# Kernel tuning notes

Measured on AMD Instinct MI355X. Metric: run time of the kernel, lower is better.

The kernel has to match this reference:

```python
import jax, jax.numpy as jnp
import numpy as np
from jax import lax

B_SZ = 2
EMBED = 384          # d_model == d_inner (expand=1)
DEPTH = 12
DSTATE = 16
DCONV = 4
DTRANK = 24          # ceil(384/16)
GH, GW, GD = 16, 8, 8
PH, PW, PD = 16, 32, 8
L = GH * GW * GD            # 1024 tokens
PATCH_DIM = PH * PW * PD    # 4096


def setup_inputs() -> dict:
    key = jax.random.key(0)
    ks = jax.random.split(key, 12)
    d = EMBED
    return {
        "x": jax.random.normal(ks[0], (B_SZ, 1, GH * PH, GW * PW, GD * PD), dtype=jnp.float32),
        "batch_params": jax.random.uniform(ks[1], (B_SZ, 4), minval=0.1, maxval=1.0),
        "patch_w": jax.random.normal(ks[2], (PATCH_DIM, d)) * 0.02,
        "patch_b": jnp.zeros((d,), jnp.float32),
        "in_proj_w": jax.random.normal(ks[3], (DEPTH, d, 2 * d)) * 0.02,
        "conv_w": jax.random.normal(ks[4], (DEPTH, d, DCONV)) * 0.1,
        "conv_b": jnp.zeros((DEPTH, d), jnp.float32),
        "x_proj_w": jax.random.normal(ks[5], (DEPTH, d, DTRANK + 2 * DSTATE)) * 0.02,
        "dt_proj_w": jax.random.normal(ks[6], (DEPTH, DTRANK, d)) * 0.02,
        "dt_proj_b": jnp.full((DEPTH, d), -4.6, jnp.float32),  # softplus(-4.6) ~ 0.01 init dt
        "A_log": jnp.log(jnp.tile(jnp.arange(1, DSTATE + 1, dtype=jnp.float32), (DEPTH, EMBED, 1))),
        "Dskip": jnp.ones((DEPTH, d), jnp.float32),
        "out_proj_w": jax.random.normal(ks[7], (DEPTH, d, d)) * 0.02,
        "norm_w": jnp.ones((DEPTH, d), jnp.float32),
        "norm_b": jnp.zeros((DEPTH, d), jnp.float32),
        "final_norm_w": jnp.ones((d,), jnp.float32),
        "final_norm_b": jnp.zeros((d,), jnp.float32),
        "has_velocity_mask": jnp.array([True, False]),
    }


def _layernorm(h, w, b, eps=1e-5):
    mu = h.mean(-1, keepdims=True)
    var = ((h - mu) ** 2).mean(-1, keepdims=True)
    return (h - mu) / jnp.sqrt(var + eps) * w + b


def _physical_coords(batch_params, mask):
    # grid indices -> physical (distance, angle, velocity/time), [B, L, 3]
    h = jnp.arange(GH, dtype=jnp.float32)[None, :, None, None]
    w = jnp.arange(GW, dtype=jnp.float32)[None, None, :, None]
    dd = jnp.arange(GD, dtype=jnp.float32)[None, None, None, :]
    rr = batch_params[:, 0][:, None, None, None]
    ar = batch_params[:, 1][:, None, None, None]
    vr = batch_params[:, 2][:, None, None, None]
    B = batch_params.shape[0]
    shape = (B, GH, GW, GD)
    dist = jnp.broadcast_to(h * rr, shape)
    angle = jnp.broadcast_to((w - GW / 2) * ar, shape)
    m = mask[:, None, None, None]
    vel = jnp.broadcast_to(jnp.where(m, (dd - GD / 2) * vr, dd * vr), shape)
    coords = jnp.stack([dist, angle, vel], axis=-1).reshape(B, -1, 3)
    # PIPE normalization
    d0 = coords[:, :, 0]
    dmax = jnp.max(d0, 1, keepdims=True)
    n0 = d0 / jnp.where(dmax == 0, 1.0, dmax)
    a = coords[:, :, 1]
    amax = jnp.max(jnp.abs(a), 1, keepdims=True)
    n1 = a / jnp.where(amax == 0, 1.0, amax)
    v = coords[:, :, 2]
    vam = jnp.max(jnp.abs(v), 1, keepdims=True)
    vam = jnp.where(vam == 0, 1.0, vam)
    vm = jnp.max(v, 1, keepdims=True)
    vm = jnp.where(vm == 0, 1.0, vm)
    n2 = jnp.where(mask[:, None], v / vam, v / vm)
    return jnp.stack([n0, n1, n2], axis=-1)


def _pos_embed(coords):
    # embed_dim % 3 == 0 and per-coord dim even -> pure sin/cos blocks
    dpc = EMBED // 3
    omega = 1.0 / (10000.0 ** (jnp.arange(dpc // 2, dtype=jnp.float32) / (dpc / 2.0)))
    embs = []
    for j in range(3):
        out = coords[:, :, j, None] * omega          # [B, L, dpc//2]
        embs.append(jnp.concatenate([jnp.sin(out), jnp.cos(out)], axis=-1))
    return jnp.concatenate(embs, axis=-1)            # [B, L, EMBED]


def _forward(x, batch_params, patch_w, patch_b, in_proj_w, conv_w, conv_b,
             x_proj_w, dt_proj_w, dt_proj_b, A_log, Dskip, out_proj_w,
             norm_w, norm_b, final_norm_w, final_norm_b, has_velocity_mask):
    B = x.shape[0]
    # 3D patch embed (conv3d with stride == kernel == patch) as reshape + GEMM
    xp = x[:, 0].reshape(B, GH, PH, GW, PW, GD, PD)
    xp = xp.transpose(0, 1, 3, 5, 2, 4, 6).reshape(B, L, PATCH_DIM)
    tok = xp @ patch_w + patch_b                     # [B, L, EMBED]
    coords = _physical_coords(batch_params, has_velocity_mask)
    tok = tok + _pos_embed(coords)

    def mamba_layer(tok, params):
        ipw, cw, cb, xpw, dtw, dtb, Al, Dp, opw, nw, nb = params
        h = _layernorm(tok, nw, nb)
        xz = h @ ipw                                  # [B, L, 2d]
        xi, z = jnp.split(xz, 2, axis=-1)
        # depthwise causal conv1d (kernel DCONV) + silu
        xc = lax.conv_general_dilated(
            xi.transpose(0, 2, 1), cw[:, None, :], (1,), [(DCONV - 1, 0)],
            feature_group_count=EMBED, dimension_numbers=("NCH", "OIH", "NCH"))
        xc = jax.nn.silu(xc + cb[:, None]).transpose(0, 2, 1)   # [B, L, d]
        dbl = xc @ xpw
        dt = jax.nn.softplus(dbl[..., :DTRANK] @ dtw + dtb)     # [B, L, d]
        Bm = dbl[..., DTRANK:DTRANK + DSTATE]                   # [B, L, N]
        Cm = dbl[..., DTRANK + DSTATE:]                         # [B, L, N]
        A = -jnp.exp(Al)                                        # [d, N]

        def step(hst, inps):
            dt_t, B_t, C_t, u_t = inps                          # [B,d],[B,N],[B,N],[B,d]
            dA = jnp.exp(dt_t[:, :, None] * A)                  # [B, d, N]
            hst = hst * dA + (dt_t * u_t)[:, :, None] * B_t[:, None, :]
            return hst, jnp.einsum("bdn,bn->bd", hst, C_t)

        h0 = jnp.zeros((B, EMBED, DSTATE), tok.dtype)
        _, ys = lax.scan(step, h0, (dt.transpose(1, 0, 2), Bm.transpose(1, 0, 2),
                                    Cm.transpose(1, 0, 2), xc.transpose(1, 0, 2)))
        y = ys.transpose(1, 0, 2) + xc * Dp
        y = y * jax.nn.silu(z)
        return tok + y @ opw, None

    tok, _ = lax.scan(mamba_layer, tok,
                      (in_proj_w, conv_w, conv_b, x_proj_w, dt_proj_w, dt_proj_b,
                       A_log, Dskip, out_proj_w, norm_w, norm_b))
    return _layernorm(tok, final_norm_w, final_norm_b)


def reference(x, batch_params, patch_w, patch_b, in_proj_w, conv_w, conv_b,
              x_proj_w, dt_proj_w, dt_proj_b, A_log, Dskip, out_proj_w,
              norm_w, norm_b, final_norm_w, final_norm_b, has_velocity_mask):
    return _forward(x, batch_params, patch_w, patch_b, in_proj_w, conv_w, conv_b,
                    x_proj_w, dt_proj_w, dt_proj_b, A_log, Dskip, out_proj_w,
                    norm_w, norm_b, final_norm_w, final_norm_b, has_velocity_mask)
```

## Files before the change

kernel.cpp:

```cpp
#include <hip/hip_runtime.h>


#define NTOK 2048

typedef short bf16x8 __attribute__((ext_vector_type(8)));
typedef float f32x4 __attribute__((ext_vector_type(4)));
typedef unsigned short us4 __attribute__((ext_vector_type(4)));

__device__ __forceinline__ float bf2f(unsigned short u) {
    return __uint_as_float(((unsigned)u) << 16);
}
__device__ __forceinline__ unsigned short f2bf(float f) {
    unsigned u = __float_as_uint(f);
    u += 0x7fffu + ((u >> 16) & 1u);
    return (unsigned short)(u >> 16);
}
__device__ __forceinline__ float siluf(float x) { return x / (1.f + expf(-x)); }

__device__ __forceinline__ float ldr(const void* p, size_t i, int bf) {
    if (bf) return bf2f(((const unsigned short*)p)[i]);
    return ((const float*)p)[i];
}
template<int BF>
__device__ __forceinline__ float ld(const void* p, size_t i) {
    if (BF) return bf2f(((const unsigned short*)p)[i]);
    return ((const float*)p)[i];
}

__global__ void detect_kernel(const void* dskip, int* flag) {
    flag[0] = (((const unsigned short*)dskip)[0] == 0x3F80u) ? 1 : 0;
}

__global__ __launch_bounds__(256)
void transposeP_kernel(const int* flag, const void* pw, unsigned short* wtP)
{
    __shared__ unsigned short Ts[32 * 36];
    const int bid = blockIdx.x;
    const int kb = bid / 12, nb = bid % 12;
    const int tid = threadIdx.x;
    const int r = tid >> 3, c0 = (tid & 7) * 4;
    const int BF = *flag;
#pragma unroll
    for (int i = 0; i < 4; i++) {
        size_t si = (size_t)(kb * 32 + r) * 384 + nb * 32 + c0 + i;
        Ts[(c0 + i) * 36 + r] = f2bf(ldr(pw, si, BF));
    }
    __syncthreads();
    *(us4*)(wtP + (size_t)(nb * 32 + r) * 4096 + kb * 32 + c0) = *(const us4*)&Ts[r * 36 + c0];
}

__global__ __launch_bounds__(256)
void transposeL_kernel(const int* flag, const void* ipw, const void* opw, int lyr,
                       unsigned short* wtL, unsigned short* wtOl)
{
    __shared__ unsigned short Ts[32 * 36];
    const int bid = blockIdx.x;
    const void* src; size_t soff; unsigned short* dst; int N, kb, nb;
    if (bid < 288) {
        src = ipw; soff = (size_t)lyr * 294912; dst = wtL; N = 768;
        kb = bid / 24; nb = bid % 24;
    } else {
        int rel = bid - 288;
        src = opw; soff = (size_t)lyr * 147456; dst = wtOl; N = 384;
        kb = rel / 12; nb = rel % 12;
    }
    const int tid = threadIdx.x;
    const int r = tid >> 3, c0 = (tid & 7) * 4;
    const int BF = *flag;
#pragma unroll
    for (int i = 0; i < 4; i++) {
        size_t si = soff + (size_t)(kb * 32 + r) * N + nb * 32 + c0 + i;
        Ts[(c0 + i) * 36 + r] = f2bf(ldr(src, si, BF));
    }
    __syncthreads();
    *(us4*)(dst + (size_t)(nb * 32 + r) * 384 + kb * 32 + c0) = *(const us4*)&Ts[r * 36 + c0];
}

__global__ __launch_bounds__(256)
void transposeAll_kernel(const int* flag, const void* ipw, const void* opw,
                         unsigned short* wtL12, unsigned short* wtO12)
{
    __shared__ unsigned short Ts[32 * 36];
    const int lyr = blockIdx.y;
    const int bid = blockIdx.x;
    const void* src; size_t soff; unsigned short* dst; int N, kb, nb;
    if (bid < 288) {
        src = ipw; soff = (size_t)lyr * 294912;
        dst = wtL12 + (size_t)lyr * 294912; N = 768;
        kb = bid / 24; nb = bid % 24;
    } else {
        int rel = bid - 288;
        src = opw; soff = (size_t)lyr * 147456;
        dst = wtO12 + (size_t)lyr * 147456; N = 384;
        kb = rel / 12; nb = rel % 12;
    }
    const int tid = threadIdx.x;
    const int r = tid >> 3, c0 = (tid & 7) * 4;
    const int BF = *flag;
#pragma unroll
    for (int i = 0; i < 4; i++) {
        size_t si = soff + (size_t)(kb * 32 + r) * N + nb * 32 + c0 + i;
        Ts[(c0 + i) * 36 + r] = f2bf(ldr(src, si, BF));
    }
    __syncthreads();
    *(us4*)(dst + (size_t)(nb * 32 + r) * 384 + kb * 32 + c0) = *(const us4*)&Ts[r * 36 + c0];
}

template<int MODE>
__global__ __launch_bounds__(256)
void gemm_kernel(const unsigned short* __restrict__ A,
                 const unsigned short* __restrict__ WT,
                 void* __restrict__ out0, unsigned short* __restrict__ out1)
{
    const int mtile = blockIdx.x;
    const int ntile = blockIdx.y;
    const int tid = threadIdx.x;
    const int w = tid >> 6, lane = tid & 63;
    const int l15 = lane & 15, quad = lane >> 4;
    const int mbase = mtile * 32;
    const int nbase = ntile * 64 + w * 16;
    f32x4 acc0 = {0.f,0.f,0.f,0.f}, acc1 = acc0;
    const bf16x8* Ap0 = (const bf16x8*)(A + (size_t)(mbase + l15) * 384 + quad * 8);
    const bf16x8* Ap1 = (const bf16x8*)(A + (size_t)(mbase + 16 + l15) * 384 + quad * 8);
    const bf16x8* Bp  = (const bf16x8*)(WT + (size_t)(nbase + l15) * 384 + quad * 8);
    const int nkt = (MODE == 1) ? 6 : 12;
    const int kt0 = (MODE == 1) ? blockIdx.z * 6 : 0;
#pragma unroll
    for (int ki = 0; ki < nkt; ki++) {
        const int kt = kt0 + ki;
        bf16x8 a0 = Ap0[kt * 4];
        bf16x8 a1 = Ap1[kt * 4];
        bf16x8 b  = Bp[kt * 4];
        acc0 = __builtin_amdgcn_mfma_f32_16x16x32_bf16(a0, b, acc0, 0, 0, 0);
        acc1 = __builtin_amdgcn_mfma_f32_16x16x32_bf16(a1, b, acc1, 0, 0, 0);
    }
    f32x4 accs[2] = {acc0, acc1};
#pragma unroll
    for (int mi = 0; mi < 2; mi++)
#pragma unroll
    for (int r = 0; r < 4; r++) {
        int m = mbase + mi * 16 + quad * 4 + r;
        int n = nbase + l15;
        float v = accs[mi][r];
        if (MODE == 0) {
            if (n < 384) ((unsigned short*)out0)[(size_t)m * 384 + n] = f2bf(v);
            else out1[(size_t)m * 384 + (n - 384)] = f2bf(siluf(v));
        } else {
            atomicAdd(&((float*)out0)[(size_t)m * 384 + n], v);
        }
    }
}

template<int BF>
__device__ void posinit_body(const void* __restrict__ pb, const void* __restrict__ bparams,
                             const unsigned char* __restrict__ maskp, float* __restrict__ tok)
{
    const int gid = blockIdx.x * 256 + threadIdx.x;
    const int t = gid / 384;
    const int n = gid - t * 384;
    const int b = t >> 10, l = t & 1023;
    const int gh = l >> 6, gw = (l >> 3) & 7, gd = l & 7;
    const int j = n >> 7;
    const int ii = n & 127;
    const int i0 = (ii < 64) ? ii : ii - 64;
    const float omega = exp2f(-(float)i0 * 0.20762050593046014f);
    float rr = ld<BF>(bparams, b * 4 + 0);
    float ar = ld<BF>(bparams, b * 4 + 1);
    float vr = ld<BF>(bparams, b * 4 + 2);
    bool mk = maskp[b] != 0;
    float cj;
    if (j == 0) {
        float dmax = (rr >= 0.f) ? 15.f * rr : 0.f;
        if (dmax == 0.f) dmax = 1.f;
        cj = (float)gh * rr / dmax;
    } else if (j == 1) {
        float amax = 4.f * fabsf(ar);
        if (amax == 0.f) amax = 1.f;
        cj = (float)(gw - 4) * ar / amax;
    } else {
        if (mk) {
            float dmx = 4.f * fabsf(vr);
            if (dmx == 0.f) dmx = 1.f;
            cj = (float)(gd - 4) * vr / dmx;
        } else {
            float dmx = (vr >= 0.f) ? 7.f * vr : 0.f;
            if (dmx == 0.f) dmx = 1.f;
            cj = (float)gd * vr / dmx;
        }
    }
    float s = cj * omega;
    float pos = (ii < 64) ? sinf(s) : cosf(s);
    tok[gid] = ld<BF>(pb, n) + pos;
}

__global__ __launch_bounds__(256)
void posinit_kernel(const int* flag, const void* pb, const void* bparams,
                    const unsigned char* maskp, float* tok)
{
    if (*flag) posinit_body<1>(pb, bparams, maskp, tok);
    else       posinit_body<0>(pb, bparams, maskp, tok);
}

template<int BF>
__device__ void patch_body(const void* __restrict__ x,
                           const unsigned short* __restrict__ WT,
                           float* __restrict__ tok, short* __restrict__ As)
{
    const int mtile = blockIdx.x;
    const int ntile = blockIdx.y;
    const int kz = blockIdx.z;
    const int tid = threadIdx.x;
    const int w = tid >> 6, lane = tid & 63;
    const int l15 = lane & 15, quad = lane >> 4;
    const int nbase = ntile * 64 + (w >> 1) * 32;
    const int mrow0 = (w & 1) * 32 + l15;
    const int bb0 = mtile >> 4, gh0 = mtile & 15;
    f32x4 acc00 = {0.f,0.f,0.f,0.f}, acc01 = acc00, acc10 = acc00, acc11 = acc00;
#pragma unroll
    for (int p2 = 0; p2 < 4; p2++) {
        const int plane = kz * 4 + p2;
        if (p2) __syncthreads();
        {
            const size_t sbase = (size_t)bb0 * 4194304u + (size_t)gh0 * 262144u
                               + (size_t)plane * 16384u;
#pragma unroll
            for (int it = 0; it < 16; it++) {
                int e = it * 1024 + tid * 4;
                int gw = e >> 11, pw = (e >> 6) & 31, gd = (e >> 3) & 7, pd = e & 7;
                short* dst = As + (gw * 8 + gd) * 260 + pw * 8 + pd;
                if (BF) {
                    *(us4*)dst = *(const us4*)((const unsigned short*)x + sbase + e);
                } else {
                    float4 p4 = *(const float4*)((const float*)x + sbase + e);
                    dst[0] = (short)f2bf(p4.x); dst[1] = (short)f2bf(p4.y);
                    dst[2] = (short)f2bf(p4.z); dst[3] = (short)f2bf(p4.w);
                }
            }
        }
        __syncthreads();
        const bf16x8* Bp0 = (const bf16x8*)(WT + (size_t)(nbase + l15) * 4096
                                            + plane * 256 + quad * 8);
        const bf16x8* Bp1 = (const bf16x8*)(WT + (size_t)(nbase + 16 + l15) * 4096
                                            + plane * 256 + quad * 8);
#pragma unroll
        for (int kt = 0; kt < 8; kt++) {
            const short* a0p = As + mrow0 * 260 + kt * 32 + quad * 8;
            const short* a1p = a0p + 16 * 260;
            bf16x8 a0, a1;
            {
                us4 lo = *(const us4*)a0p, hi = *(const us4*)(a0p + 4);
                a0[0]=lo[0]; a0[1]=lo[1]; a0[2]=lo[2]; a0[3]=lo[3];
                a0[4]=hi[0]; a0[5]=hi[1]; a0[6]=hi[2]; a0[7]=hi[3];
                us4 lo1 = *(const us4*)a1p, hi1 = *(const us4*)(a1p + 4);
                a1[0]=lo1[0]; a1[1]=lo1[1]; a1[2]=lo1[2]; a1[3]=lo1[3];
                a1[4]=hi1[0]; a1[5]=hi1[1]; a1[6]=hi1[2]; a1[7]=hi1[3];
            }
            bf16x8 b0 = Bp0[kt * 4];
            bf16x8 b1 = Bp1[kt * 4];
            acc00 = __builtin_amdgcn_mfma_f32_16x16x32_bf16(a0, b0, acc00, 0, 0, 0);
            acc01 = __builtin_amdgcn_mfma_f32_16x16x32_bf16(a0, b1, acc01, 0, 0, 0);
            acc10 = __builtin_amdgcn_mfma_f32_16x16x32_bf16(a1, b0, acc10, 0, 0, 0);
            acc11 = __builtin_amdgcn_mfma_f32_16x16x32_bf16(a1, b1, acc11, 0, 0, 0);
        }
    }
    f32x4 accs[2][2] = {{acc00, acc01}, {acc10, acc11}};
#pragma unroll
    for (int mi = 0; mi < 2; mi++)
#pragma unroll
    for (int ni = 0; ni < 2; ni++) {
        int n = nbase + ni * 16 + l15;
#pragma unroll
        for (int r = 0; r < 4; r++) {
            int m = mtile * 64 + (w & 1) * 32 + mi * 16 + quad * 4 + r;
            atomicAdd(&tok[(size_t)m * 384 + n], accs[mi][ni][r]);
        }
    }
}

__global__ __launch_bounds__(256)
void patch_kernel(const int* flag, const void* x, const unsigned short* wtP, float* tok)
{
    __shared__ short As[64 * 260];
    if (*flag) patch_body<1>(x, wtP, tok, As);
    else       patch_body<0>(x, wtP, tok, As);
}

__global__ __launch_bounds__(64)
void ln_kernel(const int* flag, const float* __restrict__ in, const void* __restrict__ w,
               const void* __restrict__ b, int woff, void* __restrict__ out, int obf)
{
    const int BF = *flag;
    const int wbf = obf | BF;
    const int t = blockIdx.x;
    const int lane = threadIdx.x;
    float v[6];
    float s = 0.f;
#pragma unroll
    for (int i = 0; i < 6; i++) { v[i] = in[(size_t)t * 384 + lane + 64 * i]; s += v[i]; }
#pragma unroll
    for (int o = 1; o < 64; o <<= 1) s += __shfl_xor(s, o);
    const float mu = s * (1.f / 384.f);
    float s2 = 0.f;
#pragma unroll
    for (int i = 0; i < 6; i++) { float d = v[i] - mu; s2 += d * d; }
#pragma unroll
    for (int o = 1; o < 64; o <<= 1) s2 += __shfl_xor(s2, o);
    const float rstd = rsqrtf(s2 * (1.f / 384.f) + 1e-5f);
#pragma unroll
    for (int i = 0; i < 6; i++) {
        int c = lane + 64 * i;
        float o = (v[i] - mu) * rstd * ldr(w, woff + c, BF) + ldr(b, woff + c, BF);
        if (wbf) ((unsigned short*)out)[(size_t)t * 384 + c] = f2bf(o);
        else     ((float*)out)[(size_t)t * 384 + c] = o;
    }
}

template<int BF>
__device__ void convfused_body(float* xcs, float* dblA,
                          const unsigned short* __restrict__ xi,
                          const void* __restrict__ cw, const void* __restrict__ cb,
                          const void* __restrict__ xpw, const void* __restrict__ dtw,
                          const void* __restrict__ dtbp, int lyr,
                          unsigned short* __restrict__ xc, unsigned short* __restrict__ dtv,
                          float* __restrict__ Bm, float* __restrict__ Cm)
{
    const int tb = blockIdx.x * 4;
    const int tid = threadIdx.x;
    const size_t cwo = (size_t)lyr * 1536;
    const size_t cbo = (size_t)lyr * 384;
    const size_t xpo = (size_t)lyr * 21504;
    const size_t dto = (size_t)lyr * 9216;
#pragma unroll
    for (int i = 0; i < 6; i++) {
        int p = i * 256 + tid;
        int tl = p / 384, c = p - tl * 384;
        int t = tb + tl;
        int b = t >> 10, l = t & 1023;
        float acc = ld<BF>(cb, cbo + c);
#pragma unroll
        for (int jj = 0; jj < 4; jj++) {
            int ls = l - 3 + jj;
            if (ls >= 0)
                acc = fmaf(bf2f(xi[(size_t)((b << 10) + ls) * 384 + c]),
                           ld<BF>(cw, cwo + c * 4 + jj), acc);
        }
        float s = siluf(acc);
        xcs[tl * 384 + c] = s;
        xc[(size_t)t * 384 + c] = f2bf(s);
    }
    __syncthreads();
    {
        const int tok = tid >> 6, og = tid & 63;
        const int t = tb + tok;
        if (og < 56) {
            float acc = 0.f;
            const float* xr = xcs + tok * 384;
#pragma unroll 8
            for (int k = 0; k < 384; k++)
                acc = fmaf(xr[k], ld<BF>(xpw, xpo + (size_t)k * 56 + og), acc);
            if (og < 24) dblA[tok * 24 + og] = acc;
            else if (og < 40) Bm[(size_t)t * 16 + (og - 24)] = acc;
            else Cm[(size_t)t * 16 + (og - 40)] = acc;
        }
    }
    __syncthreads();
#pragma unroll
    for (int i = 0; i < 6; i++) {
        int p = i * 256 + tid;
        int tl = p / 384, c = p - tl * 384;
        int t = tb + tl;
        float acc = ld<BF>(dtbp, cbo + c);
        const float* dr = dblA + tl * 24;
#pragma unroll
        for (int r = 0; r < 24; r++)
            acc = fmaf(dr[r], ld<BF>(dtw, dto + (size_t)r * 384 + c), acc);
        float sp = fmaxf(acc, 0.f) + log1pf(expf(-fabsf(acc)));
        dtv[(size_t)t * 384 + c] = f2bf(sp);
    }
}

__global__ __launch_bounds__(256)
void convfused_kernel(const int* flag, const unsigned short* xi, const void* cw,
                      const void* cb, const void* xpw, const void* dtw, const void* dtbp,
                      int lyr, unsigned short* xc, unsigned short* dtv,
                      float* Bm, float* Cm)
{
    __shared__ float xcs[4 * 384];
    __shared__ float dblA[4 * 24];
    if (*flag) convfused_body<1>(xcs, dblA, xi, cw, cb, xpw, dtw, dtbp, lyr, xc, dtv, Bm, Cm);
    else       convfused_body<0>(xcs, dblA, xi, cw, cb, xpw, dtw, dtbp, lyr, xc, dtv, Bm, Cm);
}

template<int BF>
__device__ void scan1_body(unsigned short* dts, unsigned short* xcs, float* Bs,
                           const unsigned short* __restrict__ dt,
                           const unsigned short* __restrict__ xc,
                           const float* __restrict__ Bm, const void* __restrict__ Alog,
                           int aoff, float* __restrict__ chA, float* __restrict__ chH)
{
    const int b = blockIdx.z, ch = blockIdx.y;
    const int tid = threadIdx.x;
    const int cl = tid >> 4;
    const int c = blockIdx.x * 16 + cl;
    const int n = tid & 15;
    const int tbase = (b << 10) + ch * 64;
    {
        const int row = tid >> 2, part = (tid & 3) * 4;
        const int c0 = blockIdx.x * 16;
        *(us4*)&dts[row * 16 + part] =
            *(const us4*)(dt + (size_t)(tbase + row) * 384 + c0 + part);
        *(us4*)&xcs[row * 16 + part] =
            *(const us4*)(xc + (size_t)(tbase + row) * 384 + c0 + part);
        *(float4*)&Bs[tid * 4] = *(const float4*)(Bm + (size_t)tbase * 16 + tid * 4);
    }
    __syncthreads();
    const float Ac = -expf(ld<BF>(Alog, (size_t)aoff + c * 16 + n));
    float h = 0.f, ap = 1.f;
#pragma unroll 4
    for (int i = 0; i < 64; i++) {
        float d = bf2f(dts[i * 16 + cl]);
        float u = bf2f(xcs[i * 16 + cl]);
        float bn = Bs[i * 16 + n];
        float dA = expf(d * Ac);
        h = fmaf(h, dA, d * u * bn);
        ap *= dA;
    }
    size_t idx = ((size_t)((b * 16 + ch) * 384 + c)) * 16 + n;
    chA[idx] = ap;
    chH[idx] = h;
}

__global__ __launch_bounds__(256)
void scan1_kernel(const int* flag, const unsigned short* dt, const unsigned short* xc,
                  const float* Bm, const void* Alog, int aoff, float* chA, float* chH)
{
    __shared__ unsigned short dts[1024];
    __shared__ unsigned short xcs[1024];
    __shared__ float Bs[1024];
    if (*flag) scan1_body<1>(dts, xcs, Bs, dt, xc, Bm, Alog, aoff, chA, chH);
    else       scan1_body<0>(dts, xcs, Bs, dt, xc, Bm, Alog, aoff, chA, chH);
}

template<int BF>
__device__ void scan2_body(unsigned short* dts, unsigned short* xcs, unsigned short* zss,
                           float* Bs, float* Cs,
                           const unsigned short* __restrict__ dt,
                           const unsigned short* __restrict__ xc,
                           const float* __restrict__ Bm, const float* __restrict__ Cm,
                           const unsigned short* __restrict__ zs,
                           const void* __restrict__ Alog, const void* __restrict__ Dp,
                           int aoff, int doff,
                           const float* __restrict__ chA, const float* __restrict__ chH,
                           unsigned short* __restrict__ y)
{
    const int b = blockIdx.z, ch = blockIdx.y;
    const int tid = threadIdx.x;
    const int cl = tid >> 4;
    const int c = blockIdx.x * 16 + cl;
    const int n = tid & 15;
    const int tbase = (b << 10) + ch * 64;
    {
        const int row = tid >> 2, part = (tid & 3) * 4;
        const int c0 = blockIdx.x * 16;
        *(us4*)&dts[row * 16 + part] =
            *(const us4*)(dt + (size_t)(tbase + row) * 384 + c0 + part);
        *(us4*)&xcs[row * 16 + part] =
            *(const us4*)(xc + (size_t)(tbase + row) * 384 + c0 + part);
        *(us4*)&zss[row * 16 + part] =
            *(const us4*)(zs + (size_t)(tbase + row) * 384 + c0 + part);
        *(float4*)&Bs[tid * 4] = *(const float4*)(Bm + (size_t)tbase * 16 + tid * 4);
        *(float4*)&Cs[tid * 4] = *(const float4*)(Cm + (size_t)tbase * 16 + tid * 4);
    }
    const float Ac = -expf(ld<BF>(Alog, (size_t)aoff + c * 16 + n));
    const float dp = ld<BF>(Dp, (size_t)doff + c);
    float h = 0.f;
    for (int c2 = 0; c2 < ch; c2++) {
        size_t i2 = ((size_t)((b * 16 + c2) * 384 + c)) * 16 + n;
        h = fmaf(chA[i2], h, chH[i2]);
    }
    __syncthreads();
#pragma unroll 4
    for (int i = 0; i < 64; i++) {
        float d = bf2f(dts[i * 16 + cl]);
        float u = bf2f(xcs[i * 16 + cl]);
        float bn = Bs[i * 16 + n];
        float cn = Cs[i * 16 + n];
        float dA = expf(d * Ac);
        h = fmaf(h, dA, d * u * bn);
        float p = h * cn;
        p += __shfl_xor(p, 1);
        p += __shfl_xor(p, 2);
        p += __shfl_xor(p, 4);
        p += __shfl_xor(p, 8);
        if (n == 0) {
            int t = tbase + i;
            y[(size_t)t * 384 + c] = f2bf((p + u * dp) * bf2f(zss[i * 16 + cl]));
        }
    }
}

__global__ __launch_bounds__(256)
void scan2_kernel(const int* flag, const unsigned short* dt, const unsigned short* xc,
                  const float* Bm, const float* Cm, const unsigned short* zs,
                  const void* Alog, const void* Dp, int aoff, int doff,
                  const float* chA, const float* chH, unsigned short* y)
{
    __shared__ unsigned short dts[1024];
    __shared__ unsigned short xcs[1024];
    __shared__ unsigned short zss[1024];
    __shared__ float Bs[1024];
    __shared__ float Cs[1024];
    if (*flag) scan2_body<1>(dts, xcs, zss, Bs, Cs, dt, xc, Bm, Cm, zs, Alog, Dp,
                             aoff, doff, chA, chH, y);
    else       scan2_body<0>(dts, xcs, zss, Bs, Cs, dt, xc, Bm, Cm, zs, Alog, Dp,
                             aoff, doff, chA, chH, y);
}

extern "C" void kernel_launch(void* const* d_in, const int* in_sizes, int n_in,
                              void* d_out, int out_size, void* d_ws, size_t ws_size,
                              hipStream_t stream) {
    const void* x        = d_in[0];
    const void* bparams  = d_in[1];
    const void* patch_w  = d_in[2];
    const void* patch_b  = d_in[3];
    const void* in_proj  = d_in[4];
    const void* conv_w   = d_in[5];
    const void* conv_b   = d_in[6];
    const void* x_proj   = d_in[7];
    const void* dt_w     = d_in[8];
    const void* dt_b     = d_in[9];
    const void* A_log    = d_in[10];
    const void* Dskip    = d_in[11];
    const void* out_proj = d_in[12];
    const void* norm_w   = d_in[13];
    const void* norm_b   = d_in[14];
    const void* fnw      = d_in[15];
    const void* fnb      = d_in[16];
    const unsigned char* maskp = (const unsigned char*)d_in[17];

    const size_t TD = (size_t)NTOK * 384;
    char* p = (char*)d_ws;
    float* tok = (float*)p;              p += TD * 4;
    unsigned short* hbuf = (unsigned short*)p; p += TD * 2;
    unsigned short* xi   = (unsigned short*)p; p += TD * 2;
    unsigned short* zs   = (unsigned short*)p; p += TD * 2;
    unsigned short* xc   = (unsigned short*)p; p += TD * 2;
    unsigned short* dtb_ = (unsigned short*)p; p += TD * 2;
    float* Bmb = (float*)p;              p += (size_t)NTOK * 16 * 4;
    float* Cmb = (float*)p;              p += (size_t)NTOK * 16 * 4;
    float* chA = (float*)p;              p += 196608 * 4;
    float* chH = (float*)p;              p += 196608 * 4;
    int* dflag = (int*)p;                p += 256;
    unsigned short* wbase = (unsigned short*)p;
    const size_t fixed = (size_t)(p - (char*)d_ws);
    const int big = (ws_size >= fixed + (size_t)(12 * 294912 + 12 * 147456) * 2 + 4096);

    unsigned short* wtP   = wbase;
    unsigned short* wtL12 = wbase;
    unsigned short* wtO12 = wbase + (size_t)12 * 294912;
    unsigned short* wtLs  = wbase + (size_t)1572864;
    unsigned short* wtOs  = wtLs + (size_t)294912;
    unsigned short* yb    = hbuf;

    detect_kernel<<<1, 1, 0, stream>>>(Dskip, dflag);
    transposeP_kernel<<<1536, 256, 0, stream>>>(dflag, patch_w, wtP);
    posinit_kernel<<<3072, 256, 0, stream>>>(dflag, patch_b, bparams, maskp, tok);
    patch_kernel<<<dim3(32, 6, 4), 256, 0, stream>>>(dflag, x, wtP, tok);
    if (big)
        transposeAll_kernel<<<dim3(432, 12), 256, 0, stream>>>(dflag, in_proj, out_proj,
                                                               wtL12, wtO12);

    for (int lyr = 0; lyr < 12; lyr++) {
        unsigned short *wtL, *wtO;
        if (big) {
            wtL = wtL12 + (size_t)lyr * 294912;
            wtO = wtO12 + (size_t)lyr * 147456;
        } else {
            transposeL_kernel<<<432, 256, 0, stream>>>(dflag, in_proj, out_proj, lyr,
                                                       wtLs, wtOs);
            wtL = wtLs; wtO = wtOs;
        }
        ln_kernel<<<NTOK, 64, 0, stream>>>(dflag, tok, norm_w, norm_b, lyr * 384, hbuf, 1);
        gemm_kernel<0><<<dim3(64, 12), 256, 0, stream>>>(hbuf, wtL, xi, zs);
        convfused_kernel<<<NTOK / 4, 256, 0, stream>>>(
            dflag, xi, conv_w, conv_b, x_proj, dt_w, dt_b, lyr, xc, dtb_, Bmb, Cmb);
        scan1_kernel<<<dim3(24, 16, 2), 256, 0, stream>>>(
            dflag, dtb_, xc, Bmb, A_log, lyr * 384 * 16, chA, chH);
        scan2_kernel<<<dim3(24, 16, 2), 256, 0, stream>>>(
            dflag, dtb_, xc, Bmb, Cmb, zs, A_log, Dskip, lyr * 384 * 16, lyr * 384,
            chA, chH, yb);
        gemm_kernel<1><<<dim3(64, 6, 2), 256, 0, stream>>>(yb, wtO, tok, nullptr);
    }

    ln_kernel<<<NTOK, 64, 0, stream>>>(dflag, tok, fnw, fnb, 0, d_out, 0);
}
```

Baseline: 1.242 ms.

## Fuse layernorm into in-projection GEMM and enlarge out-projection GEMM tiles

Each in-projection GEMM block now computes layernorm for its 32 token rows, writes the bf16 result into shared memory and feeds the MFMA loop from there. This removes the separate ln_kernel launch and the hbuf round trip. The cost is that layernorm is recomputed in every one of the 12 N-tile blocks. The out-projection GEMM now gives each wave a 32x32 tile instead of 32x16, halving the M-block count and reusing A/B fragments across four MFMAs.

```diff
diff --git a/kernel.cpp b/kernel.cpp
--- a/kernel.cpp
+++ b/kernel.cpp
@@ -106,31 +106,107 @@
     *(us4*)(dst + (size_t)(nb * 32 + r) * 384 + kb * 32 + c0) = *(const us4*)&Ts[r * 36 + c0];
 }
 
-template<int MODE>
-__global__ __launch_bounds__(256)
-void gemm_kernel(const unsigned short* __restrict__ A,
-                 const unsigned short* __restrict__ WT,
-                 void* __restrict__ out0, unsigned short* __restrict__ out1)
+__global__ __launch_bounds__(256)
+void gemm1_kernel(const unsigned short* __restrict__ A,
+                  const unsigned short* __restrict__ WT,
+                  float* __restrict__ out0)
 {
     const int mtile = blockIdx.x;
     const int ntile = blockIdx.y;
     const int tid = threadIdx.x;
     const int w = tid >> 6, lane = tid & 63;
     const int l15 = lane & 15, quad = lane >> 4;
-    const int mbase = mtile * 32;
-    const int nbase = ntile * 64 + w * 16;
-    f32x4 acc0 = {0.f,0.f,0.f,0.f}, acc1 = acc0;
+    const int mbase = mtile * 64 + (w & 1) * 32;
+    const int nbase = ntile * 64 + (w >> 1) * 32;
+    f32x4 acc00 = {0.f,0.f,0.f,0.f}, acc01 = acc00, acc10 = acc00, acc11 = acc00;
     const bf16x8* Ap0 = (const bf16x8*)(A + (size_t)(mbase + l15) * 384 + quad * 8);
     const bf16x8* Ap1 = (const bf16x8*)(A + (size_t)(mbase + 16 + l15) * 384 + quad * 8);
-    const bf16x8* Bp  = (const bf16x8*)(WT + (size_t)(nbase + l15) * 384 + quad * 8);
-    const int nkt = (MODE == 1) ? 6 : 12;
-    const int kt0 = (MODE == 1) ? blockIdx.z * 6 : 0;
-#pragma unroll
-    for (int ki = 0; ki < nkt; ki++) {
+    const bf16x8* Bp0 = (const bf16x8*)(WT + (size_t)(nbase + l15) * 384 + quad * 8);
+    const bf16x8* Bp1 = (const bf16x8*)(WT + (size_t)(nbase + 16 + l15) * 384 + quad * 8);
+    const int kt0 = blockIdx.z * 6;
+#pragma unroll
+    for (int ki = 0; ki < 6; ki++) {
         const int kt = kt0 + ki;
         bf16x8 a0 = Ap0[kt * 4];
         bf16x8 a1 = Ap1[kt * 4];
-        bf16x8 b  = Bp[kt * 4];
+        bf16x8 b0 = Bp0[kt * 4];
+        bf16x8 b1 = Bp1[kt * 4];
+        acc00 = __builtin_amdgcn_mfma_f32_16x16x32_bf16(a0, b0, acc00, 0, 0, 0);
+        acc01 = __builtin_amdgcn_mfma_f32_16x16x32_bf16(a0, b1, acc01, 0, 0, 0);
+        acc10 = __builtin_amdgcn_mfma_f32_16x16x32_bf16(a1, b0, acc10, 0, 0, 0);
+        acc11 = __builtin_amdgcn_mfma_f32_16x16x32_bf16(a1, b1, acc11, 0, 0, 0);
+    }
+    f32x4 accs[2][2] = {{acc00, acc01}, {acc10, acc11}};
+#pragma unroll
+    for (int mi = 0; mi < 2; mi++)
+#pragma unroll
+    for (int ni = 0; ni < 2; ni++)
+#pragma unroll
+    for (int r = 0; r < 4; r++) {
+        int m = mbase + mi * 16 + quad * 4 + r;
+        int n = nbase + ni * 16 + l15;
+        atomicAdd(&out0[(size_t)m * 384 + n], accs[mi][ni][r]);
+    }
+}
+
+__global__ __launch_bounds__(256)
+void lngemm_kernel(const int* flag, const float* __restrict__ tok,
+                   const void* __restrict__ nw, const void* __restrict__ nb, int woff,
+                   const unsigned short* __restrict__ WT,
+                   unsigned short* __restrict__ xi, unsigned short* __restrict__ zs)
+{
+    __shared__ short As[32 * 392];
+    const int BF = *flag;
+    const int mtile = blockIdx.x;
+    const int ntile = blockIdx.y;
+    const int tid = threadIdx.x;
+    const int w = tid >> 6, lane = tid & 63;
+    const int l15 = lane & 15, quad = lane >> 4;
+    {
+        const int row = tid >> 3, oct = tid & 7;
+        const float* src = tok + (size_t)(mtile * 32 + row) * 384 + oct * 48;
+        float4 v[12];
+        float s = 0.f, s2 = 0.f;
+#pragma unroll
+        for (int j = 0; j < 12; j++) {
+            v[j] = ((const float4*)src)[j];
+            s  += v[j].x + v[j].y + v[j].z + v[j].w;
+            s2 += v[j].x * v[j].x + v[j].y * v[j].y + v[j].z * v[j].z + v[j].w * v[j].w;
+        }
+        s  += __shfl_xor(s, 1);  s  += __shfl_xor(s, 2);  s  += __shfl_xor(s, 4);
+        s2 += __shfl_xor(s2, 1); s2 += __shfl_xor(s2, 2); s2 += __shfl_xor(s2, 4);
+        const float mu = s * (1.f / 384.f);
+        const float rstd = rsqrtf(fmaxf(s2 * (1.f / 384.f) - mu * mu, 0.f) + 1e-5f);
+        short* dst = As + row * 392 + oct * 48;
+#pragma unroll
+        for (int j = 0; j < 12; j++) {
+            int c = woff + oct * 48 + j * 4;
+            us4 o;
+            o[0] = f2bf((v[j].x - mu) * rstd * ldr(nw, c + 0, BF) + ldr(nb, c + 0, BF));
+            o[1] = f2bf((v[j].y - mu) * rstd * ldr(nw, c + 1, BF) + ldr(nb, c + 1, BF));
+            o[2] = f2bf((v[j].z - mu) * rstd * ldr(nw, c + 2, BF) + ldr(nb, c + 2, BF));
+            o[3] = f2bf((v[j].w - mu) * rstd * ldr(nw, c + 3, BF) + ldr(nb, c + 3, BF));
+            *(us4*)(dst + j * 4) = o;
+        }
+    }
+    __syncthreads();
+    const int nbase = ntile * 64 + w * 16;
+    f32x4 acc0 = {0.f,0.f,0.f,0.f}, acc1 = acc0;
+    const bf16x8* Bp = (const bf16x8*)(WT + (size_t)(nbase + l15) * 384 + quad * 8);
+#pragma unroll
+    for (int kt = 0; kt < 12; kt++) {
+        const short* a0p = As + l15 * 392 + kt * 32 + quad * 8;
+        const short* a1p = a0p + 16 * 392;
+        bf16x8 a0, a1;
+        {
+            us4 lo = *(const us4*)a0p, hi = *(const us4*)(a0p + 4);
+            a0[0]=lo[0]; a0[1]=lo[1]; a0[2]=lo[2]; a0[3]=lo[3];
+            a0[4]=hi[0]; a0[5]=hi[1]; a0[6]=hi[2]; a0[7]=hi[3];
+            us4 lo1 = *(const us4*)a1p, hi1 = *(const us4*)(a1p + 4);
+            a1[0]=lo1[0]; a1[1]=lo1[1]; a1[2]=lo1[2]; a1[3]=lo1[3];
+            a1[4]=hi1[0]; a1[5]=hi1[1]; a1[6]=hi1[2]; a1[7]=hi1[3];
+        }
+        bf16x8 b = Bp[kt * 4];
         acc0 = __builtin_amdgcn_mfma_f32_16x16x32_bf16(a0, b, acc0, 0, 0, 0);
         acc1 = __builtin_amdgcn_mfma_f32_16x16x32_bf16(a1, b, acc1, 0, 0, 0);
     }
@@ -139,15 +215,11 @@
     for (int mi = 0; mi < 2; mi++)
 #pragma unroll
     for (int r = 0; r < 4; r++) {
-        int m = mbase + mi * 16 + quad * 4 + r;
+        int m = mtile * 32 + mi * 16 + quad * 4 + r;
         int n = nbase + l15;
         float v = accs[mi][r];
-        if (MODE == 0) {
-            if (n < 384) ((unsigned short*)out0)[(size_t)m * 384 + n] = f2bf(v);
-            else out1[(size_t)m * 384 + (n - 384)] = f2bf(siluf(v));
-        } else {
-            atomicAdd(&((float*)out0)[(size_t)m * 384 + n], v);
-        }
+        if (n < 384) xi[(size_t)m * 384 + n] = f2bf(v);
+        else zs[(size_t)m * 384 + (n - 384)] = f2bf(siluf(v));
     }
 }
 
@@ -580,8 +652,8 @@
                                                        wtLs, wtOs);
             wtL = wtLs; wtO = wtOs;
         }
-        ln_kernel<<<NTOK, 64, 0, stream>>>(dflag, tok, norm_w, norm_b, lyr * 384, hbuf, 1);
-        gemm_kernel<0><<<dim3(64, 12), 256, 0, stream>>>(hbuf, wtL, xi, zs);
+        lngemm_kernel<<<dim3(64, 12), 256, 0, stream>>>(
+            dflag, tok, norm_w, norm_b, lyr * 384, wtL, xi, zs);
         convfused_kernel<<<NTOK / 4, 256, 0, stream>>>(
             dflag, xi, conv_w, conv_b, x_proj, dt_w, dt_b, lyr, xc, dtb_, Bmb, Cmb);
         scan1_kernel<<<dim3(24, 16, 2), 256, 0, stream>>>(
@@ -589,7 +661,7 @@
         scan2_kernel<<<dim3(24, 16, 2), 256, 0, stream>>>(
             dflag, dtb_, xc, Bmb, Cmb, zs, A_log, Dskip, lyr * 384 * 16, lyr * 384,
             chA, chH, yb);
-        gemm_kernel<1><<<dim3(64, 6, 2), 256, 0, stream>>>(yb, wtO, tok, nullptr);
+        gemm1_kernel<<<dim3(32, 6, 2), 256, 0, stream>>>(yb, wtO, tok);
     }
 
     ln_kernel<<<NTOK, 64, 0, stream>>>(dflag, tok, fnw, fnb, 0, d_out, 0);
```

Result: slower. 1.307 ms (+5.3%).
